# Performance work log

Measured on AMD Instinct MI355X. Metric: run time of the kernel, lower is better.

## Reference

```python
import jax, jax.numpy as jnp
import numpy as np

REG_MAX = 16
NC = 80
TOPK = 10
ALPHA = 0.5
BETA = 6.0
IMG = 640.0
EPS = 1e-7
BOX_W, CLS_W, DFL_W = 7.5, 0.5, 1.5


def make_anchors():
    anchors, strides = [], []
    for s, size in [(8, 80), (16, 40), (32, 20)]:
        yy, xx = jnp.meshgrid(jnp.arange(size, dtype=jnp.float32), jnp.arange(size, dtype=jnp.float32), indexing='ij')
        xy = (jnp.stack([xx, yy], -1).reshape(-1, 2) + 0.5) * s
        anchors.append(xy)
        strides.append(jnp.full((size * size,), float(s), jnp.float32))
    return jnp.concatenate(anchors), jnp.concatenate(strides)  # [A,2], [A]


def pairwise_iou(gt, pd, eps=EPS):
    # gt [B,G,4], pd [B,A,4] -> [B,G,A]
    b1 = gt[:, :, None, :]
    b2 = pd[:, None, :, :]
    inter = jnp.clip(jnp.minimum(b1[..., 2:], b2[..., 2:]) - jnp.maximum(b1[..., :2], b2[..., :2]), 0.0).prod(-1)
    a1 = (b1[..., 2:] - b1[..., :2]).prod(-1)
    a2 = (b2[..., 2:] - b2[..., :2]).prod(-1)
    return inter / (a1 + a2 - inter + eps)


def ciou(b1, b2, eps=EPS):
    # elementwise CIoU on [...,4] xyxy boxes
    inter = jnp.clip(jnp.minimum(b1[..., 2:], b2[..., 2:]) - jnp.maximum(b1[..., :2], b2[..., :2]), 0.0).prod(-1)
    area1 = jnp.maximum(b1[..., 2:] - b1[..., :2], eps).prod(-1)
    area2 = jnp.maximum(b2[..., 2:] - b2[..., :2], eps).prod(-1)
    union = area1 + area2 - inter + eps
    iou = inter / union
    cw = jnp.maximum(b1[..., 2], b2[..., 2]) - jnp.minimum(b1[..., 0], b2[..., 0])
    ch = jnp.maximum(b1[..., 3], b2[..., 3]) - jnp.minimum(b1[..., 1], b2[..., 1])
    c2 = cw * cw + ch * ch + eps
    c1c = (b1[..., :2] + b1[..., 2:]) * 0.5
    c2c = (b2[..., :2] + b2[..., 2:]) * 0.5
    rho2 = ((c1c - c2c) ** 2).sum(-1)
    w1 = jnp.maximum(b1[..., 2] - b1[..., 0], eps)
    h1 = jnp.maximum(b1[..., 3] - b1[..., 1], eps)
    w2 = jnp.maximum(b2[..., 2] - b2[..., 0], eps)
    h2 = jnp.maximum(b2[..., 3] - b2[..., 1], eps)
    v = (4.0 / jnp.pi ** 2) * (jnp.arctan(w2 / h2) - jnp.arctan(w1 / h1)) ** 2
    alpha = jax.lax.stop_gradient(v / (1.0 - iou + v + eps))
    return jnp.clip(iou - (rho2 / c2 + v * alpha), -1.0, 1.0)


def assign(pd_scores, pd_bboxes, gt_labels, gt_bboxes, mask_gt_f):
    # TaskAlignedAssigner.forward (runs under stop_gradient at call site)
    B, A, C = pd_scores.shape
    G = gt_bboxes.shape[1]
    iou = pairwise_iou(gt_bboxes, pd_bboxes)                       # [B,G,A]
    cls_score = pd_scores.max(-1)[:, None, :] * mask_gt_f[:, :, None]
    align = (cls_score ** ALPHA) * (iou ** BETA) * mask_gt_f[:, :, None]
    k = min(TOPK, A)
    vals, idx = jax.lax.top_k(align, k)                            # [B,G,k]
    valid = (mask_gt_f[:, :, None] > 0) & (vals > 0)
    b_ix = jnp.arange(B)[:, None, None]
    g_ix = jnp.arange(G)[None, :, None]
    mask_pos = jnp.zeros((B, G, A), bool).at[b_ix, g_ix, idx].max(valid)
    fg = mask_pos.any(1)                                           # [B,A]
    miou = iou * mask_pos.astype(iou.dtype)
    matched = miou.argmax(1)                                       # [B,A]
    tlab = jnp.take_along_axis(gt_labels, matched, 1)
    tlab = jnp.clip(tlab, 0, C - 1)
    tlab = jnp.where(fg, tlab, 0)
    tbox = jnp.take_along_axis(gt_bboxes, matched[..., None], 1)   # [B,A,4]
    iou_s = jnp.take_along_axis(miou, matched[:, None, :], 1)[:, 0, :]
    tscore = jax.nn.one_hot(tlab, C, dtype=pd_scores.dtype) * iou_s[..., None] * fg[..., None].astype(pd_scores.dtype)
    return tlab, tbox, tscore, fg


def yolo_loss(pred_dist, pred_cls, gt_labels, gt_bboxes, mask_gt):
    B, A, _ = pred_dist.shape
    R = REG_MAX
    anchors, strides = make_anchors()
    # decode: DFL expectation -> pixel boxes
    prob = jax.nn.softmax(pred_dist.reshape(B, A, 4, R), -1)
    dist = (prob * jnp.arange(R, dtype=prob.dtype)).sum(-1)        # stride units
    dpix = dist * strides[None, :, None]
    ax, ay = anchors[None, :, 0], anchors[None, :, 1]
    pred_boxes = jnp.clip(jnp.stack([ax - dpix[..., 0], ay - dpix[..., 1], ax + dpix[..., 2], ay + dpix[..., 3]], -1), 0.0, IMG)
    pd_scores = jax.nn.sigmoid(pred_cls)
    mgf = mask_gt.astype(jnp.float32)
    tlab, tbox, tscore, fg = jax.tree.map(jax.lax.stop_gradient, assign(pd_scores, pred_boxes, gt_labels, gt_bboxes, mgf))
    # cls: BCE with logits, sum / max(score_sum, 1)
    x, t = pred_cls, tscore
    bce = jnp.maximum(x, 0.0) - x * t + jnp.log1p(jnp.exp(-jnp.abs(x)))
    score_sum = jnp.maximum(tscore.sum(), 1.0)
    loss_cls = bce.sum() / score_sum
    fgf = fg.astype(jnp.float32)
    num_fg = jnp.maximum(fgf.sum(), 1.0)
    # box: mean(1 - CIoU) over foreground anchors
    loss_box = ((1.0 - ciou(pred_boxes, tbox)) * fgf).sum() / num_fg
    # DFL: box2dist in stride units, bilinear CE over left/right bins
    target_ltrb = jnp.stack([ax - tbox[..., 0], ay - tbox[..., 1], tbox[..., 2] - ax, tbox[..., 3] - ay], -1) / strides[None, :, None]
    target_ltrb = jnp.clip(target_ltrb, 0.0, R - 1.01)
    tleft = jnp.clip(jnp.floor(target_ltrb).astype(jnp.int32), 0, R - 1)
    tright = jnp.clip(tleft + 1, 0, R - 1)
    wr = jnp.clip(target_ltrb - tleft.astype(target_ltrb.dtype), 0.0, 1.0)
    wl = 1.0 - wr
    logp = jax.nn.log_softmax(pred_dist.reshape(B, A, 4, R), -1)
    ll = -jnp.take_along_axis(logp, tleft[..., None], -1)[..., 0]
    lr = -jnp.take_along_axis(logp, tright[..., None], -1)[..., 0]
    dfl = (ll * wl + lr * wr).sum(-1)                              # [B,A]
    loss_dfl = (dfl * fgf).sum() / num_fg / 4.0
    return BOX_W * loss_box + CLS_W * loss_cls + DFL_W * loss_dfl


def setup_inputs() -> dict:
    key = jax.random.key(0)
    k0, k1, k2, k3, k4 = jax.random.split(key, 5)
    B, A, G = 32, 8400, 40
    pred_dist = jax.random.normal(k0, (B, A, 4 * REG_MAX), dtype=jnp.float32)
    pred_cls = jax.random.normal(k1, (B, A, NC), dtype=jnp.float32)
    gt_labels = jax.random.randint(k2, (B, G), 0, NC)
    centers = jax.random.uniform(k3, (B, G, 2), minval=60.0, maxval=580.0)
    wh = jax.random.uniform(k4, (B, G, 2), minval=10.0, maxval=100.0)
    gt_bboxes = jnp.concatenate([centers - wh * 0.5, centers + wh * 0.5], -1).astype(jnp.float32)
    mask_gt = jnp.ones((B, G), dtype=bool)
    return {"pred_dist": pred_dist, "pred_cls": pred_cls, "gt_labels": gt_labels, "gt_bboxes": gt_bboxes, "mask_gt": mask_gt}


def reference(pred_dist, pred_cls, gt_labels, gt_bboxes, mask_gt):
    return yolo_loss(pred_dist, pred_cls, gt_labels, gt_bboxes, mask_gt)
```

## Files before the change

### kernel.cpp

```cpp
#include <hip/hip_runtime.h>
#include <cmath>


namespace {

constexpr int B = 32;
constexpr int A = 8400;
constexpr int G = 40;
constexpr int C = 80;
constexpr float EPS = 1e-7f;
constexpr float IMG = 640.0f;

__device__ __forceinline__ void anchor_of(int a, float& ax, float& ay, float& st) {
  int x, y;
  if (a < 6400)      { x = a % 80; y = a / 80; st = 8.0f; }
  else if (a < 8000) { int t = a - 6400; x = t % 40; y = t / 40; st = 16.0f; }
  else               { int t = a - 8000; x = t % 20; y = t / 20; st = 32.0f; }
  ax = ((float)x + 0.5f) * st;
  ay = ((float)y + 0.5f) * st;
}

__global__ __launch_bounds__(256) void k_pre(
    const float* __restrict__ pred_dist, const float* __restrict__ pred_cls,
    float* __restrict__ pbox, float* __restrict__ msqrt, double* __restrict__ acc) {
  int t = threadIdx.x;
  int lane = t & 63, wid = t >> 6;
  int g = t >> 2, j = t & 3;
  int i = blockIdx.x * 64 + g;
  int a = i % A;
  float ax, ay, st;
  anchor_of(a, ax, ay, st);

  const float4* crow = reinterpret_cast<const float4*>(pred_cls) + (size_t)i * 20;
  float mx = -3.4e38f;
  float sp = 0.f;
#pragma unroll
  for (int q = 0; q < 5; ++q) {
    float4 v = crow[j + 4 * q];
    float xs[4] = {v.x, v.y, v.z, v.w};
#pragma unroll
    for (int e = 0; e < 4; ++e) {
      float x = xs[e];
      mx = fmaxf(mx, x);
      sp += fmaxf(x, 0.f) + __logf(1.f + __expf(-fabsf(x)));
    }
  }
  mx = fmaxf(mx, __shfl_xor(mx, 1));
  mx = fmaxf(mx, __shfl_xor(mx, 2));

  const float4* drow = reinterpret_cast<const float4*>(pred_dist) + (size_t)i * 16;
  float4 w0 = drow[4 * j], w1 = drow[4 * j + 1], w2 = drow[4 * j + 2], w3 = drow[4 * j + 3];
  float xx[16] = {w0.x, w0.y, w0.z, w0.w, w1.x, w1.y, w1.z, w1.w,
                  w2.x, w2.y, w2.z, w2.w, w3.x, w3.y, w3.z, w3.w};
  float m = xx[0];
#pragma unroll
  for (int e = 1; e < 16; ++e) m = fmaxf(m, xx[e]);
  float se = 0.f, sj = 0.f;
#pragma unroll
  for (int e = 0; e < 16; ++e) {
    float ee = __expf(xx[e] - m);
    se += ee;
    sj += ee * (float)e;
  }
  float d = sj / se;
  int base = lane & ~3;
  float d0 = __shfl(d, base), d1 = __shfl(d, base + 1);
  float d2 = __shfl(d, base + 2), d3 = __shfl(d, base + 3);
  if (j == 0) {
    float4 ob;
    ob.x = fminf(fmaxf(ax - d0 * st, 0.f), IMG);
    ob.y = fminf(fmaxf(ay - d1 * st, 0.f), IMG);
    ob.z = fminf(fmaxf(ax + d2 * st, 0.f), IMG);
    ob.w = fminf(fmaxf(ay + d3 * st, 0.f), IMG);
    reinterpret_cast<float4*>(pbox)[i] = ob;
    float sg = 1.f / (1.f + __expf(-mx));
    msqrt[i] = sqrtf(sg);
  }

  double v = (double)sp;
#pragma unroll
  for (int off = 32; off; off >>= 1) v += __shfl_xor(v, off);
  __shared__ double shb[4];
  if (lane == 0) shb[wid] = v;
  __syncthreads();
  if (t == 0) {
    double s = shb[0] + shb[1] + shb[2] + shb[3];
    atomicAdd(&acc[0 * 8 + (blockIdx.x & 7)], s);
  }
}

__global__ __launch_bounds__(256) void k_topk(
    const float* __restrict__ pbox, const float* __restrict__ msqrt,
    const float* __restrict__ gt_bboxes, unsigned long long* __restrict__ mask) {
  int bg = blockIdx.x;
  int b = bg / G, g = bg % G;
  int t = threadIdx.x, lane = t & 63, wid = t >> 6;
  const float* gp = gt_bboxes + (size_t)bg * 4;
  float gx1 = gp[0], gy1 = gp[1], gx2 = gp[2], gy2 = gp[3];
  float garea = (gx2 - gx1) * (gy2 - gy1);
  const float4* pb = reinterpret_cast<const float4*>(pbox) + (size_t)b * A;
  const float* ms = msqrt + (size_t)b * A;

  float lv[10];
  int li[10];
#pragma unroll
  for (int s = 0; s < 10; ++s) { lv[s] = -1.f; li[s] = 0x40000000; }

  for (int a = t; a < A; a += 256) {
    float4 p = pb[a];
    float iw = fmaxf(fminf(gx2, p.z) - fmaxf(gx1, p.x), 0.f);
    float ih = fmaxf(fminf(gy2, p.w) - fmaxf(gy1, p.y), 0.f);
    float inter = iw * ih;
    float parea = (p.z - p.x) * (p.w - p.y);
    float iou = inter / (garea + parea - inter + EPS);
    float i2 = iou * iou;
    float v = ms[a] * i2 * i2 * i2;
    if (v > lv[9] || (v == lv[9] && a < li[9])) {
      float cv = v; int ci = a;
#pragma unroll
      for (int s = 0; s < 10; ++s) {
        bool bt = (cv > lv[s]) || (cv == lv[s] && ci < li[s]);
        float tv = bt ? cv : lv[s]; int ti = bt ? ci : li[s];
        cv = bt ? lv[s] : cv; ci = bt ? li[s] : ci;
        lv[s] = tv; li[s] = ti;
      }
    }
  }

  __shared__ float swv[4];
  __shared__ int swi[4];
  __shared__ float sbv;
  __shared__ int sbi;
  int ptr = 0;
  unsigned long long* mrow = mask + (size_t)b * A;
  for (int k = 0; k < 10; ++k) {
    float hv = lv[0]; int hi = li[0];
#pragma unroll
    for (int s = 1; s < 10; ++s) { bool sel = (ptr == s); hv = sel ? lv[s] : hv; hi = sel ? li[s] : hi; }
    if (ptr > 9) { hv = -2.f; hi = -1; }
    float rv = hv; int ri = hi;
#pragma unroll
    for (int off = 32; off; off >>= 1) {
      float ov = __shfl_xor(rv, off); int oi = __shfl_xor(ri, off);
      if (ov > rv || (ov == rv && oi < ri)) { rv = ov; ri = oi; }
    }
    if (lane == 0) { swv[wid] = rv; swi[wid] = ri; }
    __syncthreads();
    if (t == 0) {
      float bv = swv[0]; int bi = swi[0];
#pragma unroll
      for (int w = 1; w < 4; ++w)
        if (swv[w] > bv || (swv[w] == bv && swi[w] < bi)) { bv = swv[w]; bi = swi[w]; }
      sbv = bv; sbi = bi;
      if (bv > 0.f) atomicOr(&mrow[bi], 1ull << g);
    }
    __syncthreads();
    if (sbv <= 0.f) break;
    if (hi == sbi) ptr++;
  }
}

__device__ __forceinline__ float ciou_f(float4 p, float t0, float t1, float t2, float t3) {
  float iw = fmaxf(fminf(p.z, t2) - fmaxf(p.x, t0), 0.f);
  float ih = fmaxf(fminf(p.w, t3) - fmaxf(p.y, t1), 0.f);
  float inter = iw * ih;
  float w1 = fmaxf(p.z - p.x, EPS), h1 = fmaxf(p.w - p.y, EPS);
  float w2 = fmaxf(t2 - t0, EPS), h2 = fmaxf(t3 - t1, EPS);
  float uni = w1 * h1 + w2 * h2 - inter + EPS;
  float iou = inter / uni;
  float cw = fmaxf(p.z, t2) - fminf(p.x, t0);
  float ch = fmaxf(p.w, t3) - fminf(p.y, t1);
  float c2 = cw * cw + ch * ch + EPS;
  float dx = (p.x + p.z) * 0.5f - (t0 + t2) * 0.5f;
  float dy = (p.y + p.w) * 0.5f - (t1 + t3) * 0.5f;
  float rho2 = dx * dx + dy * dy;
  float dat = atanf(w2 / h2) - atanf(w1 / h1);
  const float c4pi2 = (float)(4.0 / (M_PI * M_PI));
  float v = c4pi2 * dat * dat;
  float alpha = v / (1.0f - iou + v + EPS);
  float r = iou - (rho2 / c2 + v * alpha);
  return fminf(fmaxf(r, -1.f), 1.f);
}

__device__ __forceinline__ float wave_sum(float v) {
#pragma unroll
  for (int off = 32; off; off >>= 1) v += __shfl_xor(v, off);
  return v;
}

__global__ __launch_bounds__(256) void k_loss(
    const float* __restrict__ pred_dist, const float* __restrict__ pred_cls,
    const int* __restrict__ gt_labels, const float* __restrict__ gt_bboxes,
    const float* __restrict__ pbox, const unsigned long long* __restrict__ mask,
    double* __restrict__ acc) {
  int t = threadIdx.x, lane = t & 63, wid = t >> 6;
  int i = blockIdx.x * 256 + t;
  int b = i / A, a = i - b * A;
  unsigned long long mk = mask[i];
  float corr = 0.f, sc = 0.f, nfg = 0.f, box = 0.f, dfl = 0.f;
  if (mk) {
    float4 p = reinterpret_cast<const float4*>(pbox)[i];
    float parea = (p.z - p.x) * (p.w - p.y);
    float best = 0.f;
    int bestg = -1;
    unsigned long long mm = mk;
    while (mm) {
      int g = __ffsll((unsigned long long)mm) - 1;
      mm &= mm - 1;
      const float* gp = gt_bboxes + (size_t)(b * G + g) * 4;
      float gx1 = gp[0], gy1 = gp[1], gx2 = gp[2], gy2 = gp[3];
      float iw = fmaxf(fminf(gx2, p.z) - fmaxf(gx1, p.x), 0.f);
      float ih = fmaxf(fminf(gy2, p.w) - fmaxf(gy1, p.y), 0.f);
      float inter = iw * ih;
      float garea = (gx2 - gx1) * (gy2 - gy1);
      float iou = inter / (garea + parea - inter + EPS);
      if (iou > best) { best = iou; bestg = g; }
    }
    if (bestg >= 0) {
      sc = best;
      nfg = 1.f;
      int lab = gt_labels[b * G + bestg];
      lab = lab < 0 ? 0 : (lab > C - 1 ? C - 1 : lab);
      float xl = pred_cls[(size_t)i * C + lab];
      corr = -xl * best;
      const float* gp = gt_bboxes + (size_t)(b * G + bestg) * 4;
      float t0 = gp[0], t1 = gp[1], t2 = gp[2], t3 = gp[3];
      box = 1.0f - ciou_f(p, t0, t1, t2, t3);
      float ax, ay, st;
      anchor_of(a, ax, ay, st);
      float rst = 1.f / st;
      float tgt[4] = {(ax - t0) * rst, (ay - t1) * rst, (t2 - ax) * rst, (t3 - ay) * rst};
      const float4* dr = reinterpret_cast<const float4*>(pred_dist) + (size_t)i * 16;
      const float* drf = pred_dist + (size_t)i * 64;
#pragma unroll
      for (int l = 0; l < 4; ++l) {
        float4 u0 = dr[4 * l], u1 = dr[4 * l + 1], u2 = dr[4 * l + 2], u3 = dr[4 * l + 3];
        float xs[16] = {u0.x, u0.y, u0.z, u0.w, u1.x, u1.y, u1.z, u1.w,
                        u2.x, u2.y, u2.z, u2.w, u3.x, u3.y, u3.z, u3.w};
        float m = xs[0];
#pragma unroll
        for (int e = 1; e < 16; ++e) m = fmaxf(m, xs[e]);
        float se = 0.f;
#pragma unroll
        for (int e = 0; e < 16; ++e) se += __expf(xs[e] - m);
        float lse = m + __logf(se);
        float tt = fminf(fmaxf(tgt[l], 0.f), 14.99f);
        int tl = (int)tt;
        float wr = tt - (float)tl;
        float wl = 1.f - wr;
        float xa = drf[l * 16 + tl];
        float xb = drf[l * 16 + tl + 1];
        dfl += (lse - xa) * wl + (lse - xb) * wr;
      }
    }
  }
  float s0 = wave_sum(corr), s1 = wave_sum(sc), s2 = wave_sum(nfg);
  float s3 = wave_sum(box), s4 = wave_sum(dfl);
  __shared__ float sh[4][5];
  if (lane == 0) { sh[wid][0] = s0; sh[wid][1] = s1; sh[wid][2] = s2; sh[wid][3] = s3; sh[wid][4] = s4; }
  __syncthreads();
  if (t == 0) {
    double a0 = 0, a1 = 0, a2 = 0, a3 = 0, a4 = 0;
#pragma unroll
    for (int w = 0; w < 4; ++w) {
      a0 += sh[w][0]; a1 += sh[w][1]; a2 += sh[w][2]; a3 += sh[w][3]; a4 += sh[w][4];
    }
    if (a2 != 0.0) {
      int slot = blockIdx.x & 7;
      atomicAdd(&acc[0 * 8 + slot], a0);
      atomicAdd(&acc[1 * 8 + slot], a1);
      atomicAdd(&acc[2 * 8 + slot], a2);
      atomicAdd(&acc[3 * 8 + slot], a3);
      atomicAdd(&acc[4 * 8 + slot], a4);
    }
  }
}

__global__ void k_final(const double* __restrict__ acc, float* __restrict__ out) {
  double q[5];
#pragma unroll
  for (int j = 0; j < 5; ++j) {
    double s = 0;
#pragma unroll
    for (int w = 0; w < 8; ++w) s += acc[j * 8 + w];
    q[j] = s;
  }
  double bce = q[0];
  double scs = fmax(q[1], 1.0);
  double nf = fmax(q[2], 1.0);
  double loss = 7.5 * (q[3] / nf) + 0.5 * (bce / scs) + 1.5 * (q[4] / nf / 4.0);
  out[0] = (float)loss;
}

}

extern "C" void kernel_launch(void* const* d_in, const int* in_sizes, int n_in,
                              void* d_out, int out_size, void* d_ws, size_t ws_size,
                              hipStream_t stream) {
  (void)in_sizes; (void)n_in; (void)out_size; (void)ws_size;
  const float* pred_dist = (const float*)d_in[0];
  const float* pred_cls  = (const float*)d_in[1];
  const int*   gt_labels = (const int*)d_in[2];
  const float* gt_bboxes = (const float*)d_in[3];

  unsigned long long* mask = (unsigned long long*)d_ws;
  double* acc  = (double*)((char*)d_ws + (size_t)B * A * 8);
  float*  pbox = (float*)((char*)d_ws + (size_t)B * A * 8 + 64 * 8);
  float*  msqrt = pbox + (size_t)B * A * 4;
  float*  out = (float*)d_out;

  hipMemsetAsync(d_ws, 0, (size_t)B * A * 8 + 64 * 8, stream);
  hipLaunchKernelGGL(k_pre, dim3(B * A / 64), dim3(256), 0, stream,
                     pred_dist, pred_cls, pbox, msqrt, acc);
  hipLaunchKernelGGL(k_topk, dim3(B * G), dim3(256), 0, stream,
                     pbox, msqrt, gt_bboxes, mask);
  hipLaunchKernelGGL(k_loss, dim3(B * A / 256), dim3(256), 0, stream,
                     pred_dist, pred_cls, gt_labels, gt_bboxes, pbox, mask, acc);
  hipLaunchKernelGGL(k_final, dim3(1), dim3(1), 0, stream, acc, out);
}
```

Measured before the change: 264.9 us.

## Process two anchors per thread in k_pre, fuse mask zeroing, batch softplus logs

```diff
diff --git a/kernel.cpp b/kernel.cpp
--- a/kernel.cpp
+++ b/kernel.cpp
@@ -20,64 +20,100 @@
   ay = ((float)y + 0.5f) * st;
 }
 
-__global__ __launch_bounds__(256) void k_pre(
-    const float* __restrict__ pred_dist, const float* __restrict__ pred_cls,
-    float* __restrict__ pbox, float* __restrict__ msqrt, double* __restrict__ acc) {
-  int t = threadIdx.x;
-  int lane = t & 63, wid = t >> 6;
-  int g = t >> 2, j = t & 3;
-  int i = blockIdx.x * 64 + g;
-  int a = i % A;
-  float ax, ay, st;
-  anchor_of(a, ax, ay, st);
-
-  const float4* crow = reinterpret_cast<const float4*>(pred_cls) + (size_t)i * 20;
-  float mx = -3.4e38f;
-  float sp = 0.f;
+__device__ __forceinline__ void cls_part(const float4* c, float& sp, float& mx) {
+  float relu = 0.f, p0 = 1.f, p1 = 1.f;
+  mx = -3.4e38f;
 #pragma unroll
   for (int q = 0; q < 5; ++q) {
-    float4 v = crow[j + 4 * q];
-    float xs[4] = {v.x, v.y, v.z, v.w};
+    float xs[4] = {c[q].x, c[q].y, c[q].z, c[q].w};
 #pragma unroll
     for (int e = 0; e < 4; ++e) {
       float x = xs[e];
       mx = fmaxf(mx, x);
-      sp += fmaxf(x, 0.f) + __logf(1.f + __expf(-fabsf(x)));
-    }
-  }
-  mx = fmaxf(mx, __shfl_xor(mx, 1));
-  mx = fmaxf(mx, __shfl_xor(mx, 2));
-
-  const float4* drow = reinterpret_cast<const float4*>(pred_dist) + (size_t)i * 16;
-  float4 w0 = drow[4 * j], w1 = drow[4 * j + 1], w2 = drow[4 * j + 2], w3 = drow[4 * j + 3];
-  float xx[16] = {w0.x, w0.y, w0.z, w0.w, w1.x, w1.y, w1.z, w1.w,
-                  w2.x, w2.y, w2.z, w2.w, w3.x, w3.y, w3.z, w3.w};
-  float m = xx[0];
-#pragma unroll
-  for (int e = 1; e < 16; ++e) m = fmaxf(m, xx[e]);
+      relu += fmaxf(x, 0.f);
+      float ee = __expf(-fabsf(x));
+      if (q < 3) p0 *= (1.f + ee); else p1 *= (1.f + ee);
+    }
+  }
+  sp = relu + 0.69314718056f * (__log2f(p0) + __log2f(p1));
+}
+
+__device__ __forceinline__ float dist_expect(float4 w0, float4 w1, float4 w2, float4 w3) {
+  float x[16] = {w0.x, w0.y, w0.z, w0.w, w1.x, w1.y, w1.z, w1.w,
+                 w2.x, w2.y, w2.z, w2.w, w3.x, w3.y, w3.z, w3.w};
+  float m = x[0];
+#pragma unroll
+  for (int e = 1; e < 16; ++e) m = fmaxf(m, x[e]);
   float se = 0.f, sj = 0.f;
 #pragma unroll
   for (int e = 0; e < 16; ++e) {
-    float ee = __expf(xx[e] - m);
+    float ee = __expf(x[e] - m);
     se += ee;
     sj += ee * (float)e;
   }
-  float d = sj / se;
-  int base = lane & ~3;
-  float d0 = __shfl(d, base), d1 = __shfl(d, base + 1);
-  float d2 = __shfl(d, base + 2), d3 = __shfl(d, base + 3);
+  return sj / se;
+}
+
+__global__ __launch_bounds__(256) void k_pre(
+    const float* __restrict__ pred_dist, const float* __restrict__ pred_cls,
+    float* __restrict__ pbox, float* __restrict__ msqrt,
+    unsigned long long* __restrict__ mask, double* __restrict__ acc) {
+  int t = threadIdx.x, lane = t & 63, wid = t >> 6, j = t & 3, g = t >> 2;
+  int base = blockIdx.x * 128;
+  int i0 = base + g, i1 = base + 64 + g;
+
+  const float4* cls4 = reinterpret_cast<const float4*>(pred_cls);
+  const float4* dst4 = reinterpret_cast<const float4*>(pred_dist);
+
+  float4 c0[5], c1[5], d0[4], d1[4];
+#pragma unroll
+  for (int q = 0; q < 5; ++q) c0[q] = cls4[(size_t)i0 * 20 + j + 4 * q];
+#pragma unroll
+  for (int q = 0; q < 5; ++q) c1[q] = cls4[(size_t)i1 * 20 + j + 4 * q];
+#pragma unroll
+  for (int r = 0; r < 4; ++r) d0[r] = dst4[(size_t)i0 * 16 + 4 * j + r];
+#pragma unroll
+  for (int r = 0; r < 4; ++r) d1[r] = dst4[(size_t)i1 * 16 + 4 * j + r];
+
+  float sp0, mx0, sp1, mx1;
+  cls_part(c0, sp0, mx0);
+  cls_part(c1, sp1, mx1);
+  mx0 = fmaxf(mx0, __shfl_xor(mx0, 1)); mx0 = fmaxf(mx0, __shfl_xor(mx0, 2));
+  mx1 = fmaxf(mx1, __shfl_xor(mx1, 1)); mx1 = fmaxf(mx1, __shfl_xor(mx1, 2));
+
+  float de0 = dist_expect(d0[0], d0[1], d0[2], d0[3]);
+  float de1 = dist_expect(d1[0], d1[1], d1[2], d1[3]);
+  int qb = lane & ~3;
+  float e00 = __shfl(de0, qb), e01 = __shfl(de0, qb + 1),
+        e02 = __shfl(de0, qb + 2), e03 = __shfl(de0, qb + 3);
+  float e10 = __shfl(de1, qb), e11 = __shfl(de1, qb + 1),
+        e12 = __shfl(de1, qb + 2), e13 = __shfl(de1, qb + 3);
+
   if (j == 0) {
+    float ax, ay, st;
+    int a0 = i0 % A;
+    anchor_of(a0, ax, ay, st);
     float4 ob;
-    ob.x = fminf(fmaxf(ax - d0 * st, 0.f), IMG);
-    ob.y = fminf(fmaxf(ay - d1 * st, 0.f), IMG);
-    ob.z = fminf(fmaxf(ax + d2 * st, 0.f), IMG);
-    ob.w = fminf(fmaxf(ay + d3 * st, 0.f), IMG);
-    reinterpret_cast<float4*>(pbox)[i] = ob;
-    float sg = 1.f / (1.f + __expf(-mx));
-    msqrt[i] = sqrtf(sg);
-  }
-
-  double v = (double)sp;
+    ob.x = fminf(fmaxf(ax - e00 * st, 0.f), IMG);
+    ob.y = fminf(fmaxf(ay - e01 * st, 0.f), IMG);
+    ob.z = fminf(fmaxf(ax + e02 * st, 0.f), IMG);
+    ob.w = fminf(fmaxf(ay + e03 * st, 0.f), IMG);
+    reinterpret_cast<float4*>(pbox)[i0] = ob;
+    msqrt[i0] = sqrtf(1.f / (1.f + __expf(-mx0)));
+    mask[i0] = 0ull;
+
+    int a1 = i1 % A;
+    anchor_of(a1, ax, ay, st);
+    ob.x = fminf(fmaxf(ax - e10 * st, 0.f), IMG);
+    ob.y = fminf(fmaxf(ay - e11 * st, 0.f), IMG);
+    ob.z = fminf(fmaxf(ax + e12 * st, 0.f), IMG);
+    ob.w = fminf(fmaxf(ay + e13 * st, 0.f), IMG);
+    reinterpret_cast<float4*>(pbox)[i1] = ob;
+    msqrt[i1] = sqrtf(1.f / (1.f + __expf(-mx1)));
+    mask[i1] = 0ull;
+  }
+
+  double v = (double)sp0 + (double)sp1;
 #pragma unroll
   for (int off = 32; off; off >>= 1) v += __shfl_xor(v, off);
   __shared__ double shb[4];
@@ -104,7 +140,7 @@
   float lv[10];
   int li[10];
 #pragma unroll
-  for (int s = 0; s < 10; ++s) { lv[s] = -1.f; li[s] = 0x40000000; }
+  for (int s = 0; s < 10; ++s) { lv[s] = 0.f; li[s] = 0x7fffffff; }
 
   for (int a = t; a < A; a += 256) {
     float4 p = pb[a];
@@ -115,7 +151,7 @@
     float iou = inter / (garea + parea - inter + EPS);
     float i2 = iou * iou;
     float v = ms[a] * i2 * i2 * i2;
-    if (v > lv[9] || (v == lv[9] && a < li[9])) {
+    if (v > lv[9] || (v == lv[9] && v > 0.f && a < li[9])) {
       float cv = v; int ci = a;
 #pragma unroll
       for (int s = 0; s < 10; ++s) {
@@ -137,7 +173,7 @@
     float hv = lv[0]; int hi = li[0];
 #pragma unroll
     for (int s = 1; s < 10; ++s) { bool sel = (ptr == s); hv = sel ? lv[s] : hv; hi = sel ? li[s] : hi; }
-    if (ptr > 9) { hv = -2.f; hi = -1; }
+    if (ptr > 9) { hv = -1.f; hi = -1; }
     float rv = hv; int ri = hi;
 #pragma unroll
     for (int off = 32; off; off >>= 1) {
@@ -279,11 +315,11 @@
 __global__ void k_final(const double* __restrict__ acc, float* __restrict__ out) {
   double q[5];
 #pragma unroll
-  for (int j = 0; j < 5; ++j) {
+  for (int jj = 0; jj < 5; ++jj) {
     double s = 0;
 #pragma unroll
-    for (int w = 0; w < 8; ++w) s += acc[j * 8 + w];
-    q[j] = s;
+    for (int w = 0; w < 8; ++w) s += acc[jj * 8 + w];
+    q[jj] = s;
   }
   double bce = q[0];
   double scs = fmax(q[1], 1.0);
@@ -309,9 +345,9 @@
   float*  msqrt = pbox + (size_t)B * A * 4;
   float*  out = (float*)d_out;
 
-  hipMemsetAsync(d_ws, 0, (size_t)B * A * 8 + 64 * 8, stream);
-  hipLaunchKernelGGL(k_pre, dim3(B * A / 64), dim3(256), 0, stream,
-                     pred_dist, pred_cls, pbox, msqrt, acc);
+  hipMemsetAsync(acc, 0, 64 * 8, stream);
+  hipLaunchKernelGGL(k_pre, dim3(B * A / 128), dim3(256), 0, stream,
+                     pred_dist, pred_cls, pbox, msqrt, mask, acc);
   hipLaunchKernelGGL(k_topk, dim3(B * G), dim3(256), 0, stream,
                      pbox, msqrt, gt_bboxes, mask);
   hipLaunchKernelGGL(k_loss, dim3(B * A / 256), dim3(256), 0, stream,
```

Result: faster. 255.9 us (-3.4%).
